# Kernel tuning notes

Measured on AMD Instinct MI355X. Metric: run time of the kernel, lower is better.

## Reference

```python
import jax, jax.numpy as jnp
import numpy as np

M, N, D = 100000, 64, 128  # points, channels, voxel grid side


def setup_inputs() -> dict:
    key = jax.random.key(0)
    k1, k2, k3, k4, k5 = jax.random.split(key, 5)
    rng = np.random.default_rng(0)
    # unique occupied voxels in a D^3 grid (Minkowski coords are unique)
    lin = rng.choice(D ** 3, size=M, replace=False)
    coords = np.stack(np.unravel_index(lin, (D, D, D)), axis=1).astype(np.int32)
    w_scale = 0.02  # ~1/sqrt(fan_in=27*N)
    return {
        "feats": jax.random.normal(k1, (M, N), dtype=jnp.float32),
        "W1": jax.random.normal(k2, (27, N, N), dtype=jnp.float32) * w_scale,
        "b1": jax.random.normal(k3, (N,), dtype=jnp.float32) * 0.01,
        "W2": jax.random.normal(k4, (27, N, N), dtype=jnp.float32) * w_scale,
        "b2": jax.random.normal(k5, (N,), dtype=jnp.float32) * 0.01,
        "coords": jnp.asarray(coords),
        "grid_size": D,
    }


def reference(feats, W1, b1, W2, b2, coords, grid_size):
    Dg = grid_size
    m = feats.shape[0]
    # dense hash: linear voxel id -> point index (-1 if empty)
    lin = (coords[:, 0].astype(jnp.int32) * Dg + coords[:, 1]) * Dg + coords[:, 2]
    lookup = jnp.full((Dg * Dg * Dg,), -1, dtype=jnp.int32).at[lin].set(
        jnp.arange(m, dtype=jnp.int32))
    offsets = jnp.array([[i, j, k] for i in (-1, 0, 1) for j in (-1, 0, 1)
                         for k in (-1, 0, 1)], dtype=jnp.int32)  # [27,3]

    def sparse_conv(x, W, b):
        # out[u] = b + sum_k W_k^T gather(x, u+off_k); scan over 27 offsets keeps
        # only one [M,N] gathered buffer live (memory-bound gather-GEMM-scatter)
        def step(acc, wk_off):
            W_k, off = wk_off
            nc = coords + off  # [M,3]
            inb = jnp.all((nc >= 0) & (nc < Dg), axis=1)
            nlin = (nc[:, 0] * Dg + nc[:, 1]) * Dg + nc[:, 2]
            nidx = lookup[jnp.where(inb, nlin, 0)]
            valid = inb & (nidx >= 0)
            g = jnp.where(valid[:, None], x[jnp.maximum(nidx, 0)], 0.0)  # [M,N]
            return acc + g @ W_k, None
        init = jnp.zeros_like(x) + b
        out, _ = jax.lax.scan(step, init, (W, offsets))
        return out

    h = jax.nn.relu(sparse_conv(feats, W1, b1))
    return jax.nn.relu(sparse_conv(h, W2, b2))
```

## Files before the change

kernel.cpp:

```cpp
#include <hip/hip_runtime.h>
#include <hip/hip_bf16.h>
#include <cstdint>
#include <cstddef>

typedef _Float16 half8 __attribute__((ext_vector_type(8)));
typedef float floatx16 __attribute__((ext_vector_type(16)));

#define DGRID 128
#define D3 (DGRID * DGRID * DGRID)
#define WSZ (2 * 27 * 4096)

struct __attribute__((aligned(4))) I3 { int a, b, c; };

__global__ void prep(const int* __restrict__ coords, const float* __restrict__ feats,
                     const float* __restrict__ W1, const float* __restrict__ W2,
                     int* __restrict__ lookup, _Float16* __restrict__ Whf,
                     _Float16* __restrict__ h0, _Float16* __restrict__ h, int M) {
    int tid = blockIdx.x * 256 + threadIdx.x;
    if (tid < WSZ) {
        int idx = tid;
        int j = idx & 7;
        int l = (idx >> 3) & 63;
        int f = (idx >> 9) & 7;
        int kL = idx >> 12;
        int k = kL % 27, L = kL / 27;
        int kk = f & 3, ct = f >> 2;
        int c = kk * 16 + (l >> 5) * 8 + j;
        int n = ct * 32 + (l & 31);
        const float* W = L ? W2 : W1;
        Whf[idx] = (_Float16)W[k * 4096 + c * 64 + n];
        return;
    }
    tid -= WSZ;
    if (tid < M) {
        int x = coords[3 * tid], y = coords[3 * tid + 1], z = coords[3 * tid + 2];
        lookup[(x * DGRID + y) * DGRID + z] = tid;
        return;
    }
    tid -= M;
    if (tid < 64) {
        h0[(size_t)M * 64 + tid] = (_Float16)0.f;
        h[(size_t)M * 64 + tid] = (_Float16)0.f;
        return;
    }
    tid -= 64;
    if (tid < M * 8) {
        const float4* src = (const float4*)feats + (size_t)tid * 2;
        float4 f0 = src[0], f1 = src[1];
        half8 v;
        v[0] = (_Float16)f0.x; v[1] = (_Float16)f0.y;
        v[2] = (_Float16)f0.z; v[3] = (_Float16)f0.w;
        v[4] = (_Float16)f1.x; v[5] = (_Float16)f1.y;
        v[6] = (_Float16)f1.z; v[7] = (_Float16)f1.w;
        ((half8*)h0)[tid] = v;
    }
}

template <bool FIRST, bool OUT_F16>
__global__ __launch_bounds__(64, 2) void spconv(const _Float16* __restrict__ x,
                                                const _Float16* __restrict__ Whf,
                                                const float* __restrict__ bias,
                                                const int* __restrict__ coords,
                                                const int* __restrict__ lookup,
                                                int* __restrict__ nbr,
                                                void* __restrict__ outp, int M) {
    __shared__ int nvs[27 * 64];
    const int lane = threadIdx.x;
    const int lrow = lane & 31;
    const int lhalf = lane >> 5;
    const int mw = blockIdx.x * 64;

    {
        const int row = mw + lane;
        if constexpr (FIRST) {
            if (row < M) {
                int X = coords[3 * row], Y = coords[3 * row + 1], Z = coords[3 * row + 2];
                int zlo = Z - 1;
                if (zlo < 0) zlo = 0;
                if (zlo > DGRID - 3) zlo = DGRID - 3;
                const int zi = Z - zlo;
#pragma unroll
                for (int dx = -1; dx <= 1; ++dx)
#pragma unroll
                    for (int dy = -1; dy <= 1; ++dy) {
                        int nx = X + dx, ny = Y + dy;
                        int v0 = -1, v1 = -1, v2 = -1;
                        if (((unsigned)nx < DGRID) && ((unsigned)ny < DGRID)) {
                            I3 t = *(const I3*)(lookup + ((nx * DGRID + ny) * DGRID + zlo));
                            v0 = t.a; v1 = t.b; v2 = t.c;
                        }
#pragma unroll
                        for (int dz = -1; dz <= 1; ++dz) {
                            int zc = Z + dz;
                            int i = zi + dz;
                            int val = (i == 0) ? v0 : (i == 1) ? v1 : v2;
                            int nidx = M;
                            if (((unsigned)zc < DGRID) && ((unsigned)val < (unsigned)M))
                                nidx = val;
                            int k = (dx + 1) * 9 + (dy + 1) * 3 + (dz + 1);
                            nvs[k * 64 + lane] = nidx;
                            nbr[(size_t)k * M + row] = nidx;
                        }
                    }
            } else {
#pragma unroll
                for (int k = 0; k < 27; ++k) nvs[k * 64 + lane] = M;
            }
        } else {
            const int rc = row < M ? row : M - 1;
#pragma unroll
            for (int k = 0; k < 27; ++k) nvs[k * 64 + lane] = nbr[(size_t)k * M + rc];
        }
    }
    __syncthreads();

    floatx16 acc[4];
#pragma unroll
    for (int i = 0; i < 4; ++i)
#pragma unroll
        for (int j = 0; j < 16; ++j) acc[i][j] = 0.0f;

    const half8* wb = (const half8*)Whf + lane;

    auto loadB = [&](half8* dst, int k) {
#pragma unroll
        for (int f = 0; f < 8; ++f) dst[f] = wb[(k * 8 + f) * 64];
    };
    auto loadA = [&](half8* dst, int n0, int n1) {
        const half8* p0 = (const half8*)(x + (size_t)n0 * 64 + lhalf * 8);
        const half8* p1 = (const half8*)(x + (size_t)n1 * 64 + lhalf * 8);
#pragma unroll
        for (int kk = 0; kk < 4; ++kk) {
            dst[kk] = p0[kk * 2];
            dst[4 + kk] = p1[kk * 2];
        }
    };

    int nv0[4], nv1[4];
#pragma unroll
    for (int j = 0; j < 3; ++j) {
        nv0[j] = nvs[j * 64 + lrow];
        nv1[j] = nvs[j * 64 + 32 + lrow];
    }

    half8 Ar[3][8], Br[2][8];
    loadB(Br[0], 0);
    loadA(Ar[0], nv0[0], nv1[0]);
    loadA(Ar[1], nv0[1], nv1[1]);

#pragma unroll
    for (int i = 0; i < 27; ++i) {
        {
            int jn = i + 3;
            if (jn < 27) {
                nv0[jn & 3] = nvs[jn * 64 + lrow];
                nv1[jn & 3] = nvs[jn * 64 + 32 + lrow];
            }
        }
        if (i + 1 < 27) loadB(Br[(i + 1) & 1], i + 1);
        {
            int ja = i + 2;
            if (ja < 27) loadA(Ar[ja % 3], nv0[ja & 3], nv1[ja & 3]);
        }
        __builtin_amdgcn_sched_barrier(0);
        half8* A = Ar[i % 3];
        half8* B = Br[i & 1];
#pragma unroll
        for (int kk = 0; kk < 4; ++kk)
#pragma unroll
            for (int rt = 0; rt < 2; ++rt)
#pragma unroll
                for (int ct = 0; ct < 2; ++ct)
                    acc[rt * 2 + ct] = __builtin_amdgcn_mfma_f32_32x32x16_f16(
                        A[rt * 4 + kk], B[ct * 4 + kk], acc[rt * 2 + ct], 0, 0, 0);
    }

    const float bv0 = bias[lrow], bv1 = bias[32 + lrow];
#pragma unroll
    for (int rt = 0; rt < 2; ++rt)
#pragma unroll
        for (int ct = 0; ct < 2; ++ct) {
            const float bb = ct ? bv1 : bv0;
#pragma unroll
            for (int reg = 0; reg < 16; ++reg) {
                int row = (reg & 3) + 8 * (reg >> 2) + 4 * lhalf;
                int g = mw + rt * 32 + row;
                if (g < M) {
                    float v = acc[rt * 2 + ct][reg] + bb;
                    v = v > 0.f ? v : 0.f;
                    size_t off = (size_t)g * 64 + ct * 32 + lrow;
                    if constexpr (OUT_F16)
                        ((_Float16*)outp)[off] = (_Float16)v;
                    else
                        ((float*)outp)[off] = v;
                }
            }
        }
}

extern "C" void kernel_launch(void* const* d_in, const int* in_sizes, int n_in,
                              void* d_out, int out_size, void* d_ws, size_t ws_size,
                              hipStream_t stream) {
    const float* feats = (const float*)d_in[0];
    const float* W1 = (const float*)d_in[1];
    const float* b1 = (const float*)d_in[2];
    const float* W2 = (const float*)d_in[3];
    const float* b2 = (const float*)d_in[4];
    const int* coords = (const int*)d_in[5];
    const int M = in_sizes[0] / 64;

    int* lookup = (int*)d_ws;
    int* nbr = lookup + (size_t)D3;
    _Float16* h = (_Float16*)(nbr + (size_t)27 * M);
    _Float16* h0 = h + (size_t)(M + 1) * 64;
    _Float16* Whf = h0 + (size_t)(M + 1) * 64;
    size_t need = (size_t)D3 * 4 + (size_t)27 * M * 4 +
                  2 * (size_t)(M + 1) * 64 * 2 + (size_t)WSZ * 2;
    if (ws_size < need) return;

    long long pt = (long long)WSZ + M + 64 + (long long)M * 8;
    prep<<<(int)((pt + 255) / 256), 256, 0, stream>>>(coords, feats, W1, W2, lookup, Whf,
                                                      h0, h, M);

    int cb = (M + 63) / 64;
    spconv<true, true><<<cb, 64, 0, stream>>>(h0, Whf, b1, coords, lookup, nbr,
                                              (void*)h, M);
    spconv<false, false><<<cb, 64, 0, stream>>>(h, Whf + (size_t)27 * 4096, b2, coords,
                                                lookup, nbr, d_out, M);
}
```

Before: 170.3 us.

## Reorder points into spatially sorted order via 8^3 cube compaction

Adds a compaction kernel that walks the voxel grid in 8x8x8 cubes and renumbers the points in that spatial order. It rewrites the lookup table with the new indices and builds reordered coordinates, an original-id map and a reordered fp16 feature buffer. Both conv layers then run on the spatially local ordering, so neighbor gathers within a 64-row tile should hit nearby rows and improve cache reuse. The final output is scattered back through the original-id map. The cost is an extra kernel pass over the whole dense lookup grid, an atomic counter, and non-coalesced output stores.

```diff
diff --git a/kernel.cpp b/kernel.cpp
--- a/kernel.cpp
+++ b/kernel.cpp
@@ -9,13 +9,14 @@
 #define DGRID 128
 #define D3 (DGRID * DGRID * DGRID)
 #define WSZ (2 * 27 * 4096)
+#define NCUBE 4096
 
 struct __attribute__((aligned(4))) I3 { int a, b, c; };
 
-__global__ void prep(const int* __restrict__ coords, const float* __restrict__ feats,
-                     const float* __restrict__ W1, const float* __restrict__ W2,
-                     int* __restrict__ lookup, _Float16* __restrict__ Whf,
-                     _Float16* __restrict__ h0, _Float16* __restrict__ h, int M) {
+__global__ void prep0(const int* __restrict__ coords, const float* __restrict__ W1,
+                      const float* __restrict__ W2, int* __restrict__ lookup,
+                      _Float16* __restrict__ Whf, _Float16* __restrict__ h0,
+                      _Float16* __restrict__ h, int* __restrict__ counter, int M) {
     int tid = blockIdx.x * 256 + threadIdx.x;
     if (tid < WSZ) {
         int idx = tid;
@@ -41,18 +42,63 @@
     if (tid < 64) {
         h0[(size_t)M * 64 + tid] = (_Float16)0.f;
         h[(size_t)M * 64 + tid] = (_Float16)0.f;
-        return;
-    }
-    tid -= 64;
-    if (tid < M * 8) {
-        const float4* src = (const float4*)feats + (size_t)tid * 2;
-        float4 f0 = src[0], f1 = src[1];
-        half8 v;
-        v[0] = (_Float16)f0.x; v[1] = (_Float16)f0.y;
-        v[2] = (_Float16)f0.z; v[3] = (_Float16)f0.w;
-        v[4] = (_Float16)f1.x; v[5] = (_Float16)f1.y;
-        v[6] = (_Float16)f1.z; v[7] = (_Float16)f1.w;
-        ((half8*)h0)[tid] = v;
+        if (tid == 0) *counter = 0;
+    }
+}
+
+__global__ __launch_bounds__(64) void compact(const float* __restrict__ feats,
+                                              int* __restrict__ lookup,
+                                              int* __restrict__ counter,
+                                              int* __restrict__ coordsS,
+                                              int* __restrict__ oid,
+                                              _Float16* __restrict__ h0, int M) {
+    const int cube = blockIdx.x;
+    const int cx = cube >> 8, cy = (cube >> 4) & 15, cz = cube & 15;
+    const int lane = threadIdx.x;
+    const int X = cx * 8 + (lane >> 3), Y = cy * 8 + (lane & 7), Z0 = cz * 8;
+    int* p = lookup + ((X * DGRID + Y) * DGRID + Z0);
+
+    int v[8];
+#pragma unroll
+    for (int s = 0; s < 8; ++s) v[s] = p[s];
+
+    const unsigned long long lmask = ((unsigned long long)1 << lane) - 1;
+    int loff[8];
+    int run = 0;
+#pragma unroll
+    for (int s = 0; s < 8; ++s) {
+        bool val = (unsigned)v[s] < (unsigned)M;
+        unsigned long long mk = __ballot(val);
+        loff[s] = run + (int)__popcll(mk & lmask);
+        run += (int)__popcll(mk);
+    }
+    int base = 0;
+    if (lane == 0 && run > 0) base = atomicAdd(counter, run);
+    base = __shfl(base, 0);
+
+#pragma unroll
+    for (int s = 0; s < 8; ++s) {
+        if ((unsigned)v[s] < (unsigned)M) {
+            int pos = base + loff[s];
+            int org = v[s];
+            p[s] = pos;
+            oid[pos] = org;
+            coordsS[3 * pos] = X;
+            coordsS[3 * pos + 1] = Y;
+            coordsS[3 * pos + 2] = Z0 + s;
+            const float4* src = (const float4*)(feats + (size_t)org * 64);
+            _Float16* drow = h0 + (size_t)pos * 64;
+#pragma unroll
+            for (int q = 0; q < 8; ++q) {
+                float4 f0 = src[2 * q], f1 = src[2 * q + 1];
+                half8 hv;
+                hv[0] = (_Float16)f0.x; hv[1] = (_Float16)f0.y;
+                hv[2] = (_Float16)f0.z; hv[3] = (_Float16)f0.w;
+                hv[4] = (_Float16)f1.x; hv[5] = (_Float16)f1.y;
+                hv[6] = (_Float16)f1.z; hv[7] = (_Float16)f1.w;
+                *(half8*)(drow + q * 8) = hv;
+            }
+        }
     }
 }
 
@@ -60,11 +106,13 @@
 __global__ __launch_bounds__(64, 2) void spconv(const _Float16* __restrict__ x,
                                                 const _Float16* __restrict__ Whf,
                                                 const float* __restrict__ bias,
-                                                const int* __restrict__ coords,
+                                                const int* __restrict__ coordsS,
                                                 const int* __restrict__ lookup,
                                                 int* __restrict__ nbr,
+                                                const int* __restrict__ oid,
                                                 void* __restrict__ outp, int M) {
     __shared__ int nvs[27 * 64];
+    __shared__ int oids[64];
     const int lane = threadIdx.x;
     const int lrow = lane & 31;
     const int lhalf = lane >> 5;
@@ -74,7 +122,7 @@
         const int row = mw + lane;
         if constexpr (FIRST) {
             if (row < M) {
-                int X = coords[3 * row], Y = coords[3 * row + 1], Z = coords[3 * row + 2];
+                int X = coordsS[3 * row], Y = coordsS[3 * row + 1], Z = coordsS[3 * row + 2];
                 int zlo = Z - 1;
                 if (zlo < 0) zlo = 0;
                 if (zlo > DGRID - 3) zlo = DGRID - 3;
@@ -110,6 +158,7 @@
             const int rc = row < M ? row : M - 1;
 #pragma unroll
             for (int k = 0; k < 27; ++k) nvs[k * 64 + lane] = nbr[(size_t)k * M + rc];
+            oids[lane] = oid[rc];
         }
     }
     __syncthreads();
@@ -188,11 +237,13 @@
                 if (g < M) {
                     float v = acc[rt * 2 + ct][reg] + bb;
                     v = v > 0.f ? v : 0.f;
-                    size_t off = (size_t)g * 64 + ct * 32 + lrow;
-                    if constexpr (OUT_F16)
+                    if constexpr (OUT_F16) {
+                        size_t off = (size_t)g * 64 + ct * 32 + lrow;
                         ((_Float16*)outp)[off] = (_Float16)v;
-                    else
+                    } else {
+                        size_t off = (size_t)oids[rt * 32 + row] * 64 + ct * 32 + lrow;
                         ((float*)outp)[off] = v;
+                    }
                 }
             }
         }
@@ -214,17 +265,22 @@
     _Float16* h = (_Float16*)(nbr + (size_t)27 * M);
     _Float16* h0 = h + (size_t)(M + 1) * 64;
     _Float16* Whf = h0 + (size_t)(M + 1) * 64;
+    int* coordsS = (int*)(Whf + WSZ);
+    int* oid = coordsS + (size_t)3 * M;
+    int* counter = oid + (size_t)M;
     size_t need = (size_t)D3 * 4 + (size_t)27 * M * 4 +
-                  2 * (size_t)(M + 1) * 64 * 2 + (size_t)WSZ * 2;
+                  2 * (size_t)(M + 1) * 64 * 2 + (size_t)WSZ * 2 +
+                  (size_t)4 * M * 4 + 64;
     if (ws_size < need) return;
 
-    long long pt = (long long)WSZ + M + 64 + (long long)M * 8;
-    prep<<<(int)((pt + 255) / 256), 256, 0, stream>>>(coords, feats, W1, W2, lookup, Whf,
-                                                      h0, h, M);
+    long long pt = (long long)WSZ + M + 64;
+    prep0<<<(int)((pt + 255) / 256), 256, 0, stream>>>(coords, W1, W2, lookup, Whf, h0,
+                                                       h, counter, M);
+    compact<<<NCUBE, 64, 0, stream>>>(feats, lookup, counter, coordsS, oid, h0, M);
 
     int cb = (M + 63) / 64;
-    spconv<true, true><<<cb, 64, 0, stream>>>(h0, Whf, b1, coords, lookup, nbr,
+    spconv<true, true><<<cb, 64, 0, stream>>>(h0, Whf, b1, coordsS, lookup, nbr, oid,
                                               (void*)h, M);
-    spconv<false, false><<<cb, 64, 0, stream>>>(h, Whf + (size_t)27 * 4096, b2, coords,
-                                                lookup, nbr, d_out, M);
-}
+    spconv<false, false><<<cb, 64, 0, stream>>>(h, Whf + (size_t)27 * 4096, b2, coordsS,
+                                                lookup, nbr, oid, d_out, M);
+}
```

Result: slower. 238.3 us (+39.9%).
